# Kernel optimization log

Measured on AMD Instinct MI355X. Metric: run time of the kernel, lower is better.

The kernel has to match this reference:

```python
import jax, jax.numpy as jnp
import numpy as np

N = 100000
SEQ = 12
DIMS = [32, 64, 64, 32]


def _glorot(key, shape):
    fan_in, fan_out = shape[0], shape[1]
    lim = jnp.sqrt(6.0 / (fan_in + fan_out))
    return jax.random.uniform(key, shape, jnp.float32, -lim, lim)


def setup_inputs() -> dict:
    key = jax.random.key(0)
    ks = jax.random.split(key, 8)
    x = jax.random.normal(ks[0], (N, DIMS[0], 1), dtype=jnp.float32)
    spiral_indices = jax.random.randint(ks[1], (N, SEQ), 0, N)
    # SpiralConv i: Linear(SEQ * DIMS[i], DIMS[i+1])
    W0 = _glorot(ks[2], (SEQ * DIMS[0], DIMS[1]))
    b0 = jnp.zeros((DIMS[1],), jnp.float32)
    W1 = _glorot(ks[3], (SEQ * DIMS[1], DIMS[2]))
    b1 = jnp.zeros((DIMS[2],), jnp.float32)
    W2 = _glorot(ks[4], (SEQ * DIMS[2], DIMS[3]))
    b2 = jnp.zeros((DIMS[3],), jnp.float32)
    return {"x": x, "spiral_indices": spiral_indices,
            "W0": W0, "b0": b0, "W1": W1, "b1": b1, "W2": W2, "b2": b2}


def _spiral_conv(h, idx, W, b):
    # h: [N, C]; idx: [N, SEQ] -> gathered [N, SEQ, C] -> flat [N, SEQ*C]
    n = h.shape[0]
    g = jnp.take(h, idx, axis=0).reshape(n, -1)
    return g @ W + b


def reference(x, spiral_indices, W0, b0, W1, b1, W2, b2):
    h = x[..., 0]  # squeeze(-1): [N, C_in]
    h = jax.nn.elu(_spiral_conv(h, spiral_indices, W0, b0))
    h = jax.nn.elu(_spiral_conv(h, spiral_indices, W1, b1))
    h = _spiral_conv(h, spiral_indices, W2, b2)  # final_activation=False
    return h[:, :, None]
```

## Files before the change

### kernel.cpp

```cpp
#include <hip/hip_runtime.h>
#include <math.h>


typedef __bf16 bf16;
typedef bf16  bf16x4 __attribute__((ext_vector_type(4)));
typedef bf16  bf16x8 __attribute__((ext_vector_type(8)));
typedef float f32x4  __attribute__((ext_vector_type(4)));

template<int CIN, int COUT>
__device__ inline void pack_one(const float* __restrict__ W, bf16* __restrict__ BP, int e) {
    constexpr int NT = COUT / 16, CC = CIN / 32;
    const int f = e >> 9, r = e & 511, lane = r >> 3, j = r & 7;
    const int t = f % NT, cc = (f / NT) % CC, s = f / (NT * CC);
    const int col = t * 16 + (lane & 15);
    const int k   = s * CIN + cc * 32 + (lane >> 4) * 8 + j;
    BP[e] = (bf16)W[k * COUT + col];
}

__global__ __launch_bounds__(256)
void prep_all(const float* __restrict__ x, bf16* __restrict__ xb,
              const float* __restrict__ W0, const float* __restrict__ W1,
              const float* __restrict__ W2, bf16* __restrict__ B0,
              bf16* __restrict__ B1, bf16* __restrict__ B2, int n)
{
    const int gid = blockIdx.x * 256 + threadIdx.x;
    const int e = gid * 4;
    if (e < n * 32) {
        const f32x4 v = *reinterpret_cast<const f32x4*>(x + e);
        bf16x4 o = {(bf16)v[0], (bf16)v[1], (bf16)v[2], (bf16)v[3]};
        *reinterpret_cast<bf16x4*>(xb + e) = o;
    }
    if (gid < 384 * 64)                       pack_one<32, 64>(W0, B0, gid);
    else if (gid < 384 * 64 + 768 * 64)       pack_one<64, 64>(W1, B1, gid - 384 * 64);
    else if (gid < 384 * 64 + 768 * 64 + 768 * 32)
                                              pack_one<64, 32>(W2, B2, gid - 384 * 64 - 768 * 64);
}

template<int CIN, int COUT, bool ELU, typename TOUT>
__global__ __launch_bounds__(256, 5)
void spiral_mfma(const bf16* __restrict__ h, const int* __restrict__ idx,
                 const bf16* __restrict__ BP, const float* __restrict__ bias,
                 TOUT* __restrict__ out, int n)
{
    constexpr int CC  = CIN / 32;
    constexpr int NT  = COUT / 16;
    constexpr int PS  = CIN * COUT;
    constexpr int SC  = 6 / CC;
    constexpr int NCH = 12 / SC;
    constexpr int PL  = 6;

    __shared__ bf16 Bs[SC * PS];

    const int tid  = threadIdx.x;
    const int lane = tid & 63;
    const int wave = tid >> 6;
    const int m    = lane & 15;
    const int quad = lane >> 4;
    const int i0   = (blockIdx.x * 4 + wave) * 16;
    const bool valid = (i0 < n);

    const int ir = min(i0 + m, n - 1);
    const int4* ip = reinterpret_cast<const int4*>(idx + (size_t)ir * 12);
    const int4 q0 = ip[0], q1 = ip[1], q2 = ip[2];
    const int rg[12] = {q0.x,q0.y,q0.z,q0.w, q1.x,q1.y,q1.z,q1.w, q2.x,q2.y,q2.z,q2.w};

    f32x4 acc[NT] = {};

    #pragma unroll
    for (int c = 0; c < NCH; ++c) {
        if (c) __syncthreads();
        const bf16* src = BP + (size_t)c * SC * PS;
        #pragma unroll
        for (int r2 = tid; r2 < SC * PS / 8; r2 += 256)
            *reinterpret_cast<bf16x8*>(&Bs[r2 * 8]) =
                *reinterpret_cast<const bf16x8*>(&src[r2 * 8]);
        __syncthreads();

        bf16x8 a[PL];
        #pragma unroll
        for (int sl = 0; sl < SC; ++sl)
            #pragma unroll
            for (int cc = 0; cc < CC; ++cc)
                a[sl * CC + cc] = *reinterpret_cast<const bf16x8*>(
                    h + (size_t)rg[c * SC + sl] * CIN + cc * 32 + quad * 8);
        __builtin_amdgcn_sched_barrier(0);
        #pragma unroll
        for (int p = 0; p < PL; ++p)
            #pragma unroll
            for (int t = 0; t < NT; ++t) {
                const bf16x8 b = *reinterpret_cast<const bf16x8*>(
                    &Bs[(p * NT + t) * 512 + lane * 8]);
                acc[t] = __builtin_amdgcn_mfma_f32_16x16x32_bf16(a[p], b, acc[t], 0, 0, 0);
            }
    }

    if (!valid) return;

    #pragma unroll
    for (int t = 0; t < NT; ++t) {
        const int col = t * 16 + m;
        const float bv = bias[col];
        #pragma unroll
        for (int g = 0; g < 4; ++g) {
            const int row = i0 + quad * 4 + g;
            float v = acc[t][g] + bv;
            if (ELU) v = (v > 0.f) ? v : (__expf(v) - 1.f);
            out[(size_t)row * COUT + col] = (TOUT)v;
        }
    }
}

extern "C" void kernel_launch(void* const* d_in, const int* in_sizes, int n_in,
                              void* d_out, int out_size, void* d_ws, size_t ws_size,
                              hipStream_t stream) {
    const float* x   = (const float*)d_in[0];
    const int*   idx = (const int*)d_in[1];
    const float* W0  = (const float*)d_in[2];
    const float* b0  = (const float*)d_in[3];
    const float* W1  = (const float*)d_in[4];
    const float* b1  = (const float*)d_in[5];
    const float* W2  = (const float*)d_in[6];
    const float* b2  = (const float*)d_in[7];
    float* out = (float*)d_out;

    const int n = in_sizes[0] / 32;

    bf16* xb = (bf16*)d_ws;
    bf16* h1 = xb + (size_t)n * 32;
    bf16* h2 = h1 + (size_t)n * 64;
    bf16* B0 = h2 + (size_t)n * 64;
    bf16* B1 = B0 + 384 * 64;
    bf16* B2 = B1 + 768 * 64;

    const int prep_threads = n * 8;
    prep_all<<<(prep_threads + 255) / 256, dim3(256), 0, stream>>>(x, xb, W0, W1, W2, B0, B1, B2, n);

    const int grid = (n + 63) / 64;
    spiral_mfma<32, 64, true,  bf16 ><<<grid, dim3(256), 0, stream>>>(xb, idx, B0, b0, h1,  n);
    spiral_mfma<64, 64, true,  bf16 ><<<grid, dim3(256), 0, stream>>>(h1, idx, B1, b1, h2,  n);
    spiral_mfma<64, 32, false, float><<<grid, dim3(256), 0, stream>>>(h2, idx, B2, b2, out, n);
}
```

Before: 157.8 us.

## Use 512-thread blocks with larger weight chunks and 12-deep gather batches

Doubles the block to 8 waves so each weight chunk staged in shared memory is reused by twice as many rows. Chunk size is now derived from a 48KB LDS budget (CHS = 24576/PS slices, capped at 12). Each wave issues 12 outstanding row-gather loads per batch instead of 6, and those loads are nontemporal. The aim is fewer barrier rounds, fewer redundant weight copies and more memory-level parallelism on the random gathers, at the cost of larger LDS and register use that may cut occupancy.

```diff
diff --git a/kernel.cpp b/kernel.cpp
--- a/kernel.cpp
+++ b/kernel.cpp
@@ -37,26 +37,27 @@
 }
 
 template<int CIN, int COUT, bool ELU, typename TOUT>
-__global__ __launch_bounds__(256, 5)
+__global__ __launch_bounds__(512, 4)
 void spiral_mfma(const bf16* __restrict__ h, const int* __restrict__ idx,
                  const bf16* __restrict__ BP, const float* __restrict__ bias,
                  TOUT* __restrict__ out, int n)
 {
-    constexpr int CC  = CIN / 32;
-    constexpr int NT  = COUT / 16;
-    constexpr int PS  = CIN * COUT;
-    constexpr int SC  = 6 / CC;
-    constexpr int NCH = 12 / SC;
-    constexpr int PL  = 6;
+    constexpr int CC    = CIN / 32;
+    constexpr int NT    = COUT / 16;
+    constexpr int PS    = CIN * COUT;
+    constexpr int CHS   = (24576 / PS < 12) ? (24576 / PS) : 12;
+    constexpr int NCH   = 12 / CHS;
+    constexpr int BSTEP = 12 / CC;
+    constexpr int NB    = CHS / BSTEP;
 
-    __shared__ bf16 Bs[SC * PS];
+    __shared__ bf16 Bs[CHS * PS];
 
     const int tid  = threadIdx.x;
     const int lane = tid & 63;
     const int wave = tid >> 6;
     const int m    = lane & 15;
     const int quad = lane >> 4;
-    const int i0   = (blockIdx.x * 4 + wave) * 16;
+    const int i0   = (blockIdx.x * 8 + wave) * 16;
     const bool valid = (i0 < n);
 
     const int ir = min(i0 + m, n - 1);
@@ -69,29 +70,37 @@
     #pragma unroll
     for (int c = 0; c < NCH; ++c) {
         if (c) __syncthreads();
-        const bf16* src = BP + (size_t)c * SC * PS;
+        const bf16* src = BP + (size_t)c * CHS * PS;
         #pragma unroll
-        for (int r2 = tid; r2 < SC * PS / 8; r2 += 256)
+        for (int r2 = tid; r2 < CHS * PS / 8; r2 += 512)
             *reinterpret_cast<bf16x8*>(&Bs[r2 * 8]) =
                 *reinterpret_cast<const bf16x8*>(&src[r2 * 8]);
         __syncthreads();
 
-        bf16x8 a[PL];
         #pragma unroll
-        for (int sl = 0; sl < SC; ++sl)
+        for (int b = 0; b < NB; ++b) {
+            bf16x8 a[12];
             #pragma unroll
-            for (int cc = 0; cc < CC; ++cc)
-                a[sl * CC + cc] = *reinterpret_cast<const bf16x8*>(
-                    h + (size_t)rg[c * SC + sl] * CIN + cc * 32 + quad * 8);
-        __builtin_amdgcn_sched_barrier(0);
-        #pragma unroll
-        for (int p = 0; p < PL; ++p)
+            for (int sl = 0; sl < BSTEP; ++sl) {
+                const int s = c * CHS + b * BSTEP + sl;
+                #pragma unroll
+                for (int cc = 0; cc < CC; ++cc)
+                    a[sl * CC + cc] = __builtin_nontemporal_load(
+                        reinterpret_cast<const bf16x8*>(
+                            h + (size_t)rg[s] * CIN + cc * 32 + quad * 8));
+            }
+            __builtin_amdgcn_sched_barrier(0);
             #pragma unroll
-            for (int t = 0; t < NT; ++t) {
-                const bf16x8 b = *reinterpret_cast<const bf16x8*>(
-                    &Bs[(p * NT + t) * 512 + lane * 8]);
-                acc[t] = __builtin_amdgcn_mfma_f32_16x16x32_bf16(a[p], b, acc[t], 0, 0, 0);
+            for (int p = 0; p < 12; ++p) {
+                const int fr = (b * BSTEP * CC + p) * NT;
+                #pragma unroll
+                for (int t = 0; t < NT; ++t) {
+                    const bf16x8 bb = *reinterpret_cast<const bf16x8*>(
+                        &Bs[(fr + t) * 512 + lane * 8]);
+                    acc[t] = __builtin_amdgcn_mfma_f32_16x16x32_bf16(a[p], bb, acc[t], 0, 0, 0);
+                }
             }
+        }
     }
 
     if (!valid) return;
@@ -135,8 +144,8 @@
     const int prep_threads = n * 8;
     prep_all<<<(prep_threads + 255) / 256, dim3(256), 0, stream>>>(x, xb, W0, W1, W2, B0, B1, B2, n);
 
-    const int grid = (n + 63) / 64;
-    spiral_mfma<32, 64, true,  bf16 ><<<grid, dim3(256), 0, stream>>>(xb, idx, B0, b0, h1,  n);
-    spiral_mfma<64, 64, true,  bf16 ><<<grid, dim3(256), 0, stream>>>(h1, idx, B1, b1, h2,  n);
-    spiral_mfma<64, 32, false, float><<<grid, dim3(256), 0, stream>>>(h2, idx, B2, b2, out, n);
+    const int grid = (n + 127) / 128;
+    spiral_mfma<32, 64, true,  bf16 ><<<grid, dim3(512), 0, stream>>>(xb, idx, B0, b0, h1,  n);
+    spiral_mfma<64, 64, true,  bf16 ><<<grid, dim3(512), 0, stream>>>(h1, idx, B1, b1, h2,  n);
+    spiral_mfma<64, 32, false, float><<<grid, dim3(512), 0, stream>>>(h2, idx, B2, b2, out, n);
 }
```

Result: slower. 198.8 us (+26.0%).
